# Kernel optimization log

Measured on AMD Instinct MI355X. Metric: run time of the kernel, lower is better.

The kernel has to match this reference:

```python
import math
import jax, jax.numpy as jnp
import numpy as np

S, B, H = 2048, 1, 4096
NH, HD = 32, 128          # heads, head dim
ROT = HD // 2             # rotary dim per 2D-RoPE half = 64


def rotate_half(x):
    x1, x2 = jnp.split(x, 2, axis=-1)
    return jnp.concatenate([-x2, x1], axis=-1)


def rope_tables(seq_len, dim, base=10000.0):
    inv_freq = 1.0 / (base ** (jnp.arange(0, dim, 2, dtype=jnp.float32) / dim))
    freqs = jnp.arange(seq_len, dtype=jnp.float32)[:, None] * inv_freq[None, :]
    emb = jnp.concatenate([freqs, freqs], axis=-1)  # [S, dim]
    return jnp.cos(emb), jnp.sin(emb)


def apply_rope(q, k, cos, sin, pos):
    # q,k: [S,B,NH,ROT]; pos: [S,B] -> gather cos/sin per token
    c = cos[pos][:, :, None, :]  # [S,B,1,ROT]
    s = sin[pos][:, :, None, :]
    return q * c + rotate_half(q) * s, k * c + rotate_half(k) * s


def setup_inputs() -> dict:
    key = jax.random.key(0)
    ks = jax.random.split(key, 5)
    hidden_states = jax.random.normal(ks[0], (S, B, H), dtype=jnp.float32)
    pos = jnp.arange(S, dtype=jnp.int64 if jax.config.jax_enable_x64 else jnp.int32)
    position_ids = jnp.stack([pos, pos])[None]  # [B=1, 2, S]
    attention_mask = jnp.triu(jnp.ones((S, S), dtype=bool), k=1)[None, None]  # True = masked
    scale = 0.02
    wqkv = jax.random.normal(ks[1], (3 * H, H), dtype=jnp.float32) * scale
    bqkv = jax.random.normal(ks[2], (3 * H,), dtype=jnp.float32) * scale
    wdense = jax.random.normal(ks[3], (H, H), dtype=jnp.float32) * scale
    bdense = jax.random.normal(ks[4], (H,), dtype=jnp.float32) * scale
    return {"hidden_states": hidden_states, "position_ids": position_ids,
            "attention_mask": attention_mask, "wqkv": wqkv, "bqkv": bqkv,
            "wdense": wdense, "bdense": bdense, "layer_id": 1}


def reference(hidden_states, position_ids, attention_mask, wqkv, bqkv, wdense, bdense, layer_id):
    s, b, h = hidden_states.shape
    # fused QKV projection: [S,B,NH,3*HD]
    mixed = (jnp.einsum('sbh,oh->sbo', hidden_states, wqkv) + bqkv).reshape(s, b, NH, 3 * HD)
    q, k, v = jnp.split(mixed, 3, axis=-1)  # each [S,B,NH,HD]

    # 2D RoPE: split head dim in half, rotate each half with its own position ids
    q1, q2 = jnp.split(q, 2, axis=-1)
    k1, k2 = jnp.split(k, 2, axis=-1)
    cos, sin = rope_tables(s, ROT)
    pos = position_ids[:, 0, :].T       # [S,B]
    block_pos = position_ids[:, 1, :].T  # [S,B]
    q1, k1 = apply_rope(q1, k1, cos, sin, pos)
    q2, k2 = apply_rope(q2, k2, cos, sin, block_pos)
    q = jnp.concatenate([q1, q2], axis=-1)
    k = jnp.concatenate([k1, k2], axis=-1)

    # layer-scaled attention (ChatGLM style)
    coeff = float(layer_id + 1)
    q = q / (math.sqrt(HD) * coeff)
    scores = jnp.einsum('sbhd,tbhd->bhst', q, k)  # [B,NH,S,S]
    scores = jnp.where(attention_mask, jnp.float32(-10000.0), scores)
    scores = scores.astype(jnp.float32) * coeff
    probs = jax.nn.softmax(scores, axis=-1).astype(q.dtype)
    context = jnp.einsum('bhst,tbhd->sbhd', probs, v).reshape(s, b, h)

    out = jnp.einsum('sbh,oh->sbo', context, wdense) + bdense
    return out
```

## Files before the change

### kernel.cpp

```cpp
#include <hip/hip_runtime.h>

typedef unsigned short u16;
typedef unsigned int u32;
typedef __attribute__((ext_vector_type(4))) float f32x4;
typedef __attribute__((ext_vector_type(8))) short bf16x8;
typedef __attribute__((ext_vector_type(2))) unsigned int u32x2;

#define S_LEN 2048
#define NHEAD 32
#define HDD 128
#define HID 4096
#define N_QKV 12288
#define KDIM 4096
#define RS 12288

__device__ __forceinline__ u16 f2bf(float f) {
  u32 u = __builtin_bit_cast(u32, f);
  u = (u + 0x7FFFu + ((u >> 16) & 1u)) >> 16;
  return (u16)u;
}
__device__ __forceinline__ float bf2f(u16 h) {
  u32 u = ((u32)h) << 16;
  return __builtin_bit_cast(float, u);
}

__device__ __forceinline__ void gl2lds16(const void* g, void* l) {
  __builtin_amdgcn_global_load_lds(
      (const __attribute__((address_space(1))) u32*)g,
      (__attribute__((address_space(3))) u32*)l, 16, 0, 0);
}

#define FULL_BAR()                          \
  {                                         \
    asm volatile("" ::: "memory");          \
    __builtin_amdgcn_s_barrier();           \
    asm volatile("" ::: "memory");          \
  }

__global__ __launch_bounds__(256) void cvt3_kernel(const float* __restrict__ s0, u16* __restrict__ d0, int n0,
                                                   const float* __restrict__ s1, u16* __restrict__ d1, int n1,
                                                   const float* __restrict__ s2, u16* __restrict__ d2, int n2,
                                                   float* __restrict__ cos_t, float* __restrict__ sin_t) {
  int i = blockIdx.x * blockDim.x + threadIdx.x;
  if (i < S_LEN * 32) {
    int s = i >> 5, ii = i & 31;
    float invf = expf(-0.28782313662425572f * (float)ii);
    float a = (float)s * invf;
    cos_t[i] = cosf(a);
    sin_t[i] = sinf(a);
  }
  int st = gridDim.x * blockDim.x;
  int ntot = n0 + n1 + n2;
  for (; i < ntot; i += st) {
    const float* s;
    u16* d;
    int j = i;
    if (j < n0) {
      s = s0; d = d0;
    } else if (j < n0 + n1) {
      j -= n0; s = s1; d = d1;
    } else {
      j -= n0 + n1; s = s2; d = d2;
    }
    float4 v = ((const float4*)s)[j];
    u32x2 o;
    o.x = (u32)f2bf(v.x) | ((u32)f2bf(v.y) << 16);
    o.y = (u32)f2bf(v.z) | ((u32)f2bf(v.w) << 16);
    ((u32x2*)d)[j] = o;
  }
}

__global__ __launch_bounds__(256) void rope_kernel(u16* __restrict__ mixed,
                                                   const int* __restrict__ pid,
                                                   const float* __restrict__ cos_t,
                                                   const float* __restrict__ sin_t) {
  int idx = blockIdx.x * blockDim.x + threadIdx.x;
  const int total = 2 * NHEAD * S_LEN * 2 * 8;
  if (idx >= total) return;
  int j = idx & 7;
  int half = (idx >> 3) & 1;
  int s = (idx >> 4) & (S_LEN - 1);
  int h = (idx >> 15) & (NHEAD - 1);
  int qk = idx >> 20;
  int i0 = j * 4;
  int p = pid[half * S_LEN + s];
  float4 c4 = *(const float4*)(cos_t + p * 32 + i0);
  float4 s4 = *(const float4*)(sin_t + p * 32 + i0);
  u16* base = mixed + (size_t)s * RS + h * 384 + qk * 128 + half * 64 + i0;
  ushort4 x1v = *(const ushort4*)(base);
  ushort4 x2v = *(const ushort4*)(base + 32);
  float sc = qk ? 1.0f : 0.08838834764831845f;
  ushort4 o1, o2;
  {
    float x1 = bf2f(x1v.x), x2 = bf2f(x2v.x);
    o1.x = f2bf((x1 * c4.x - x2 * s4.x) * sc);
    o2.x = f2bf((x2 * c4.x + x1 * s4.x) * sc);
  }
  {
    float x1 = bf2f(x1v.y), x2 = bf2f(x2v.y);
    o1.y = f2bf((x1 * c4.y - x2 * s4.y) * sc);
    o2.y = f2bf((x2 * c4.y + x1 * s4.y) * sc);
  }
  {
    float x1 = bf2f(x1v.z), x2 = bf2f(x2v.z);
    o1.z = f2bf((x1 * c4.z - x2 * s4.z) * sc);
    o2.z = f2bf((x2 * c4.z + x1 * s4.z) * sc);
  }
  {
    float x1 = bf2f(x1v.w), x2 = bf2f(x2v.w);
    o1.w = f2bf((x1 * c4.w - x2 * s4.w) * sc);
    o2.w = f2bf((x2 * c4.w + x1 * s4.w) * sc);
  }
  *(ushort4*)(base) = o1;
  *(ushort4*)(base + 32) = o2;
}

template <int NW, int EPI>
__global__ __launch_bounds__(512, 2) void gemmK(const u16* __restrict__ A,
                                                const u16* __restrict__ B,
                                                const float* __restrict__ bias, int N, int NTt,
                                                u16* __restrict__ outb, float* __restrict__ outf) {
  constexpr int BN = 32 * NW;
  constexpr int NLB = NW / 2;
  constexpr int BSUB = BN * 64;
  constexpr int BUFSZ = 32768 + 2 * BSUB;
  __shared__ __align__(16) char lds[2][BUFSZ];

  const int tid = threadIdx.x;
  const int lane = tid & 63, w = tid >> 6;
  const int l15 = lane & 15, g = lane >> 4;
  const int wm = w >> 1, wn = w & 1;

  int perx = gridDim.x >> 3;
  int npx = perx >> 3;
  int x = blockIdx.x & 7, loc = blockIdx.x >> 3;
  int mb = loc & 7, nb = x * npx + (loc >> 3);
  const int bm = mb * 256, bn = nb * BN;

  f32x4 acc[4][NW];
  f32x4 z4 = {0.f, 0.f, 0.f, 0.f};
#pragma unroll
  for (int mi = 0; mi < 4; ++mi)
#pragma unroll
    for (int ni = 0; ni < NW; ++ni) acc[mi][ni] = z4;

  const size_t K2 = (size_t)KDIM * 2;

  const char* gA[2];
#pragma unroll
  for (int j = 0; j < 2; ++j) {
    int slot = j * 512 + tid;
    int line = slot >> 3;
    int sl = (slot & 7) ^ (line & 7);
    int row = 2 * line + (sl >> 2);
    int colb = (sl & 3) * 16;
    gA[j] = (const char*)A + (size_t)(bm + row) * K2 + colb;
  }
  const char* gB[NLB];
#pragma unroll
  for (int j = 0; j < NLB; ++j) {
    int n_ = j * 512 + tid;
    int kkj = (n_ >= 128 * NW) ? 1 : 0;
    int m_ = n_ - kkj * 128 * NW;
    int line = m_ >> 3;
    int sl = (m_ & 7) ^ (line & 7);
    int row = 2 * line + (sl >> 2);
    int colb = (sl & 3) * 16;
    gB[j] = (const char*)B + (size_t)(bn + row) * K2 + kkj * 64 + colb;
  }
  const int ldst = w * 1024;

#define ISSUE_A(t, kk)                                                        \
  {                                                                           \
    char* Lb = lds[(t) & 1] + (kk) * 16384;                                   \
    gl2lds16(gA[0] + (size_t)(t) * 128 + (kk) * 64, Lb + ldst);               \
    gl2lds16(gA[1] + (size_t)(t) * 128 + (kk) * 64, Lb + 8192 + ldst);        \
  }
#define ISSUE_B(t)                                                            \
  {                                                                           \
    char* Lb = lds[(t) & 1] + 32768;                                          \
    _Pragma("unroll")                                                         \
    for (int j = 0; j < NLB; ++j)                                             \
      gl2lds16(gB[j] + (size_t)(t) * 128, Lb + j * 8192 + ldst);              \
  }

  int offA[4], offB[2][NW];
#pragma unroll
  for (int mi = 0; mi < 4; ++mi) {
    int r = wm * 64 + mi * 16 + l15;
    int line = r >> 1;
    int sl = (((r & 1) << 2) + g) ^ (line & 7);
    offA[mi] = line * 128 + sl * 16;
  }
#pragma unroll
  for (int kk = 0; kk < 2; ++kk)
#pragma unroll
    for (int ni = 0; ni < NW; ++ni) {
      int r = wn * (16 * NW) + ni * 16 + l15;
      int line = r >> 1;
      int sl = (((r & 1) << 2) + g) ^ (line & 7);
      offB[kk][ni] = 32768 + kk * BSUB + line * 128 + sl * 16;
    }

  ISSUE_A(0, 0);
  ISSUE_B(0);
  ISSUE_A(0, 1);
  asm volatile("s_waitcnt vmcnt(2)" ::: "memory");
  FULL_BAR();

  for (int kt = 0; kt < NTt; ++kt) {
    const char* buf = lds[kt & 1];
    const bool pf = (kt + 1) < NTt;
    bf16x8 a[4], b[NW];
#pragma unroll
    for (int mi = 0; mi < 4; ++mi) a[mi] = *(const bf16x8*)(buf + offA[mi]);
#pragma unroll
    for (int ni = 0; ni < NW; ++ni) b[ni] = *(const bf16x8*)(buf + offB[0][ni]);
    if (pf) {
      ISSUE_A(kt + 1, 0);
      ISSUE_B(kt + 1);
      asm volatile("s_waitcnt vmcnt(%0)" ::"i"(2 + NLB) : "memory");
    } else {
      asm volatile("s_waitcnt vmcnt(0)" ::: "memory");
    }
    FULL_BAR();
    __builtin_amdgcn_s_setprio(1);
#pragma unroll
    for (int mi = 0; mi < 4; ++mi)
#pragma unroll
      for (int ni = 0; ni < NW; ++ni)
        acc[mi][ni] = __builtin_amdgcn_mfma_f32_16x16x32_bf16(a[mi], b[ni], acc[mi][ni], 0, 0, 0);
    __builtin_amdgcn_s_setprio(0);
#pragma unroll
    for (int mi = 0; mi < 4; ++mi) a[mi] = *(const bf16x8*)(buf + 16384 + offA[mi]);
#pragma unroll
    for (int ni = 0; ni < NW; ++ni) b[ni] = *(const bf16x8*)(buf + offB[1][ni]);
    if (pf) {
      ISSUE_A(kt + 1, 1);
      asm volatile("s_waitcnt vmcnt(2)" ::: "memory");
    }
    FULL_BAR();
    __builtin_amdgcn_s_setprio(1);
#pragma unroll
    for (int mi = 0; mi < 4; ++mi)
#pragma unroll
      for (int ni = 0; ni < NW; ++ni)
        acc[mi][ni] = __builtin_amdgcn_mfma_f32_16x16x32_bf16(a[mi], b[ni], acc[mi][ni], 0, 0, 0);
    __builtin_amdgcn_s_setprio(0);
  }
#undef ISSUE_A
#undef ISSUE_B

#pragma unroll
  for (int ni = 0; ni < NW; ++ni) {
    int n = bn + wn * (16 * NW) + ni * 16 + l15;
    float bv = bias[n];
    if (EPI == 0) {
#pragma unroll
      for (int mi = 0; mi < 4; ++mi) {
        int m0 = bm + wm * 64 + mi * 16 + 4 * g;
#pragma unroll
        for (int rr = 0; rr < 4; ++rr)
          outb[(size_t)(m0 + rr) * N + n] = f2bf(acc[mi][ni][rr] + bv);
      }
    } else {
#pragma unroll
      for (int mi = 0; mi < 4; ++mi) {
        int m0 = bm + wm * 64 + mi * 16 + 4 * g;
#pragma unroll
        for (int rr = 0; rr < 4; ++rr) outf[(size_t)(m0 + rr) * N + n] = acc[mi][ni][rr] + bv;
      }
    }
  }
}

__global__ __launch_bounds__(256) void attn_kernel(const u16* __restrict__ mixed,
                                                   u16* __restrict__ ctx) {
  __shared__ __align__(16) u16 Ksh[32 * 136];
  __shared__ __align__(16) u16 Vsh[128 * 32];
  __shared__ __align__(16) u16 Pt[4][16 * 40];

  int tid = threadIdx.x;
  int lane = tid & 63, w = tid >> 6;
  int lane15 = lane & 15, g = lane >> 4;

  int bpair = blockIdx.x & 15;
  int h = blockIdx.x >> 4;

  const u16* qp = mixed + (size_t)h * 384;
  const u16* kp = mixed + (size_t)h * 384 + 128;
  const u16* vp = mixed + (size_t)h * 384 + 256;

  int krow = tid >> 3, kc = (tid & 7) * 16;
  int a_ = tid & 15, b_ = tid >> 4;
  f32x4 z4 = {0.f, 0.f, 0.f, 0.f};

  for (int pass = 0; pass < 2; ++pass) {
    int qi = pass ? (31 - bpair) : bpair;
    int qbase = qi * 64;
    int qrow = qbase + w * 16 + lane15;
    int ntiles = 2 * qi + 2;

    bf16x8 qf[4];
    const u16* qptr = qp + (size_t)qrow * RS + g * 8;
#pragma unroll
    for (int d0 = 0; d0 < 4; ++d0) qf[d0] = *(const bf16x8*)(qptr + d0 * 32);

    f32x4 pv[8];
#pragma unroll
    for (int db = 0; db < 8; ++db) pv[db] = z4;
    float m_run = -1e30f, l_run = 0.0f;

    for (int t = 0; t < ntiles; ++t) {
      int kb0 = t * 32;
      __syncthreads();
      {
        const bf16x8* src = (const bf16x8*)(kp + (size_t)(kb0 + krow) * RS + kc);
        bf16x8 x0 = src[0], x1 = src[1];
        *(bf16x8*)(Ksh + krow * 136 + kc) = x0;
        *(bf16x8*)(Ksh + krow * 136 + kc + 8) = x1;
        int k0 = 2 * a_, d0 = 8 * b_;
        bf16x8 r0 = *(const bf16x8*)(vp + (size_t)(kb0 + k0) * RS + d0);
        bf16x8 r1 = *(const bf16x8*)(vp + (size_t)(kb0 + k0 + 1) * RS + d0);
#pragma unroll
        for (int jj = 0; jj < 8; ++jj) {
          int d = d0 + jj;
          u32 val = (u32)(u16)r0[jj] | ((u32)(u16)r1[jj] << 16);
          *(u32*)(Vsh + d * 32 + (((k0 >> 3) ^ (d & 3)) << 3) + (k0 & 7)) = val;
        }
      }
      __syncthreads();

      f32x4 sa0 = z4, sa1 = z4;
#pragma unroll
      for (int d0 = 0; d0 < 4; ++d0) {
        bf16x8 k0f = *(const bf16x8*)(Ksh + lane15 * 136 + d0 * 32 + g * 8);
        bf16x8 k1f = *(const bf16x8*)(Ksh + (16 + lane15) * 136 + d0 * 32 + g * 8);
        sa0 = __builtin_amdgcn_mfma_f32_16x16x32_bf16(k0f, qf[d0], sa0, 0, 0, 0);
        sa1 = __builtin_amdgcn_mfma_f32_16x16x32_bf16(k1f, qf[d0], sa1, 0, 0, 0);
      }
      float s[8];
#pragma unroll
      for (int rr = 0; rr < 4; ++rr) {
        int kg0 = kb0 + 4 * g + rr;
        int kg1 = kb0 + 16 + 4 * g + rr;
        s[rr] = (kg0 > qrow) ? -1e30f : sa0[rr];
        s[4 + rr] = (kg1 > qrow) ? -1e30f : sa1[rr];
      }
      float mx = s[0];
#pragma unroll
      for (int i2 = 1; i2 < 8; ++i2) mx = fmaxf(mx, s[i2]);
      mx = fmaxf(mx, __shfl_xor(mx, 16));
      mx = fmaxf(mx, __shfl_xor(mx, 32));
      float mnew = fmaxf(m_run, mx);
      float fac = exp2f((m_run - mnew) * 1.4426950408889634f);
      float p[8], psum = 0.f;
#pragma unroll
      for (int i2 = 0; i2 < 8; ++i2) {
        p[i2] = exp2f((s[i2] - mnew) * 1.4426950408889634f);
        psum += p[i2];
      }
      psum += __shfl_xor(psum, 16);
      psum += __shfl_xor(psum, 32);
      l_run = l_run * fac + psum;
      m_run = mnew;
#pragma unroll
      for (int db = 0; db < 8; ++db) pv[db] *= fac;

      u32 w0 = (u32)f2bf(p[0]) | ((u32)f2bf(p[1]) << 16);
      u32 w1 = (u32)f2bf(p[2]) | ((u32)f2bf(p[3]) << 16);
      u32 w2 = (u32)f2bf(p[4]) | ((u32)f2bf(p[5]) << 16);
      u32 w3 = (u32)f2bf(p[6]) | ((u32)f2bf(p[7]) << 16);
      u32x2 pa, pb;
      pa.x = w0; pa.y = w1; pb.x = w2; pb.y = w3;
      *(u32x2*)(&Pt[w][lane15 * 40 + 4 * g]) = pa;
      *(u32x2*)(&Pt[w][lane15 * 40 + 16 + 4 * g]) = pb;
      asm volatile("s_waitcnt lgkmcnt(0)" ::: "memory");
      bf16x8 pfrag = *(const bf16x8*)(&Pt[w][lane15 * 40 + 8 * g]);

#pragma unroll
      for (int db = 0; db < 8; ++db) {
        int d = db * 16 + lane15;
        bf16x8 vf = *(const bf16x8*)(Vsh + d * 32 + ((g ^ (d & 3)) << 3));
        pv[db] = __builtin_amdgcn_mfma_f32_16x16x32_bf16(vf, pfrag, pv[db], 0, 0, 0);
      }
    }

    float inv = 1.0f / l_run;
#pragma unroll
    for (int db = 0; db < 8; ++db) {
      ushort4 o;
      o.x = f2bf(pv[db][0] * inv);
      o.y = f2bf(pv[db][1] * inv);
      o.z = f2bf(pv[db][2] * inv);
      o.w = f2bf(pv[db][3] * inv);
      *(ushort4*)(ctx + (size_t)qrow * HID + h * HDD + db * 16 + 4 * g) = o;
    }
    __syncthreads();
  }
}

extern "C" void kernel_launch(void* const* d_in, const int* in_sizes, int n_in,
                              void* d_out, int out_size, void* d_ws, size_t ws_size,
                              hipStream_t stream) {
  const float* hidden = (const float*)d_in[0];
  const int* pid = (const int*)d_in[1];
  const float* wqkv = (const float*)d_in[3];
  const float* bqkv = (const float*)d_in[4];
  const float* wdense = (const float*)d_in[5];
  const float* bdense = (const float*)d_in[6];
  float* out = (float*)d_out;

  char* ws = (char*)d_ws;
  u16* W1 = (u16*)ws;
  u16* W2 = (u16*)(ws + 100663296);
  u16* X = (u16*)(ws + 134217728);
  u16* mixed = (u16*)(ws + 150994944);
  u16* ctx = (u16*)(ws + 201326592);
  float* cos_t = (float*)(ws + 218103808);
  float* sin_t = (float*)(ws + 218365952);

  cvt3_kernel<<<dim3(2048), dim3(256), 0, stream>>>(
      wqkv, W1, N_QKV * KDIM / 4, wdense, W2, HID * KDIM / 4, hidden, X, S_LEN * HID / 4,
      cos_t, sin_t);

  gemmK<6, 0><<<dim3(512), dim3(512), 0, stream>>>(
      X, W1, bqkv, N_QKV, 64, mixed, nullptr);

  rope_kernel<<<dim3(8192), dim3(256), 0, stream>>>(mixed, pid, cos_t, sin_t);

  attn_kernel<<<dim3(512), dim3(256), 0, stream>>>(mixed, ctx);

  gemmK<4, 1><<<dim3(256), dim3(512), 0, stream>>>(
      ctx, W2, bdense, HID, 64, nullptr, out);
}
```

Before: 500.5 us.

## Fuse RoPE into attention loads and add dedicated larger-tile QKV GEMM

Removes the standalone RoPE kernel and applies the rotary embedding (and query scaling) inside the attention kernel: queries are rotated in registers after loading, and keys are rotated while staging each tile into shared memory. The QKV projection switches to a new GEMM with 256x384 tiles, 8 waves, triple-buffered LDS and grouped block ordering, replacing the generic gemmK instance. This removes one read-modify-write pass over Q and K and one launch, and aims for more reuse per tile in the largest GEMM. In exchange, K is rotated again by every query block that reads it, and the larger tile raises register pressure and leaves fewer blocks for the grid.

```diff
diff --git a/kernel.cpp b/kernel.cpp
--- a/kernel.cpp
+++ b/kernel.cpp
@@ -70,49 +70,139 @@
   }
 }
 
-__global__ __launch_bounds__(256) void rope_kernel(u16* __restrict__ mixed,
-                                                   const int* __restrict__ pid,
-                                                   const float* __restrict__ cos_t,
-                                                   const float* __restrict__ sin_t) {
-  int idx = blockIdx.x * blockDim.x + threadIdx.x;
-  const int total = 2 * NHEAD * S_LEN * 2 * 8;
-  if (idx >= total) return;
-  int j = idx & 7;
-  int half = (idx >> 3) & 1;
-  int s = (idx >> 4) & (S_LEN - 1);
-  int h = (idx >> 15) & (NHEAD - 1);
-  int qk = idx >> 20;
-  int i0 = j * 4;
-  int p = pid[half * S_LEN + s];
-  float4 c4 = *(const float4*)(cos_t + p * 32 + i0);
-  float4 s4 = *(const float4*)(sin_t + p * 32 + i0);
-  u16* base = mixed + (size_t)s * RS + h * 384 + qk * 128 + half * 64 + i0;
-  ushort4 x1v = *(const ushort4*)(base);
-  ushort4 x2v = *(const ushort4*)(base + 32);
-  float sc = qk ? 1.0f : 0.08838834764831845f;
-  ushort4 o1, o2;
-  {
-    float x1 = bf2f(x1v.x), x2 = bf2f(x2v.x);
-    o1.x = f2bf((x1 * c4.x - x2 * s4.x) * sc);
-    o2.x = f2bf((x2 * c4.x + x1 * s4.x) * sc);
-  }
-  {
-    float x1 = bf2f(x1v.y), x2 = bf2f(x2v.y);
-    o1.y = f2bf((x1 * c4.y - x2 * s4.y) * sc);
-    o2.y = f2bf((x2 * c4.y + x1 * s4.y) * sc);
-  }
-  {
-    float x1 = bf2f(x1v.z), x2 = bf2f(x2v.z);
-    o1.z = f2bf((x1 * c4.z - x2 * s4.z) * sc);
-    o2.z = f2bf((x2 * c4.z + x1 * s4.z) * sc);
-  }
-  {
-    float x1 = bf2f(x1v.w), x2 = bf2f(x2v.w);
-    o1.w = f2bf((x1 * c4.w - x2 * s4.w) * sc);
-    o2.w = f2bf((x2 * c4.w + x1 * s4.w) * sc);
-  }
-  *(ushort4*)(base) = o1;
-  *(ushort4*)(base + 32) = o2;
+__global__ __launch_bounds__(512, 2) void gemmQ(const u16* __restrict__ A,
+                                                const u16* __restrict__ B,
+                                                const float* __restrict__ bias,
+                                                u16* __restrict__ outb) {
+  __shared__ __align__(16) char lds[3][40960];
+
+  const int tid = threadIdx.x;
+  const int lane = tid & 63, w = tid >> 6;
+  const int l15 = lane & 15, g = lane >> 4;
+  const int wm = w >> 2, wn = w & 3;
+
+  int x = blockIdx.x & 7, loc = blockIdx.x >> 3;
+  int mb = loc & 7, nb = x * 4 + (loc >> 3);
+  const int bm = mb * 256, bn = nb * 384;
+
+  f32x4 acc[8][6];
+  f32x4 z4 = {0.f, 0.f, 0.f, 0.f};
+#pragma unroll
+  for (int mi = 0; mi < 8; ++mi)
+#pragma unroll
+    for (int ni = 0; ni < 6; ++ni) acc[mi][ni] = z4;
+
+  const size_t K2 = (size_t)KDIM * 2;
+
+  const char* gA[2];
+#pragma unroll
+  for (int j = 0; j < 2; ++j) {
+    int slot = j * 512 + tid;
+    int line = slot >> 3;
+    int sl = (slot & 7) ^ (line & 7);
+    int row = 2 * line + (sl >> 2);
+    int colb = (sl & 3) * 16;
+    gA[j] = (const char*)A + (size_t)(bm + row) * K2 + colb;
+  }
+  const char* gB[3];
+#pragma unroll
+  for (int j = 0; j < 3; ++j) {
+    int slot = j * 512 + tid;
+    int line = slot >> 3;
+    int sl = (slot & 7) ^ (line & 7);
+    int row = 2 * line + (sl >> 2);
+    int colb = (sl & 3) * 16;
+    gB[j] = (const char*)B + (size_t)(bn + row) * K2 + colb;
+  }
+  const int ldst = w * 1024;
+
+#define QIA(t, bi)                                                  \
+  {                                                                 \
+    char* Lb = lds[bi];                                             \
+    gl2lds16(gA[0] + (size_t)(t) * 64, Lb + ldst);                  \
+    gl2lds16(gA[1] + (size_t)(t) * 64, Lb + 8192 + ldst);           \
+  }
+#define QIB(t, bi)                                                  \
+  {                                                                 \
+    char* Lb = lds[bi] + 16384;                                     \
+    _Pragma("unroll")                                               \
+    for (int j = 0; j < 3; ++j)                                     \
+      gl2lds16(gB[j] + (size_t)(t) * 64, Lb + j * 8192 + ldst);     \
+  }
+
+  int offA[8], offB[6];
+#pragma unroll
+  for (int mi = 0; mi < 8; ++mi) {
+    int r = wm * 128 + mi * 16 + l15;
+    int line = r >> 1;
+    int sl = (((r & 1) << 2) + g) ^ (line & 7);
+    offA[mi] = line * 128 + sl * 16;
+  }
+#pragma unroll
+  for (int ni = 0; ni < 6; ++ni) {
+    int r = wn * 96 + ni * 16 + l15;
+    int line = r >> 1;
+    int sl = (((r & 1) << 2) + g) ^ (line & 7);
+    offB[ni] = 16384 + line * 128 + sl * 16;
+  }
+
+  QIA(0, 0); QIB(0, 0);
+  QIA(1, 1); QIB(1, 1);
+  asm volatile("s_waitcnt vmcnt(5)" ::: "memory");
+  FULL_BAR();
+
+  int cur = 0, nx2 = 2;
+  for (int kt = 0; kt < 128; ++kt) {
+    const char* buf = lds[cur];
+    const bool pf = (kt + 2) < 128;
+    bf16x8 a[4], b[6];
+#pragma unroll
+    for (int mi = 0; mi < 4; ++mi) a[mi] = *(const bf16x8*)(buf + offA[mi]);
+#pragma unroll
+    for (int ni = 0; ni < 6; ++ni) b[ni] = *(const bf16x8*)(buf + offB[ni]);
+    if (pf) QIA(kt + 2, nx2);
+    FULL_BAR();
+    __builtin_amdgcn_s_setprio(1);
+#pragma unroll
+    for (int mi = 0; mi < 4; ++mi)
+#pragma unroll
+      for (int ni = 0; ni < 6; ++ni)
+        acc[mi][ni] = __builtin_amdgcn_mfma_f32_16x16x32_bf16(a[mi], b[ni], acc[mi][ni], 0, 0, 0);
+    __builtin_amdgcn_s_setprio(0);
+#pragma unroll
+    for (int mi = 0; mi < 4; ++mi) a[mi] = *(const bf16x8*)(buf + offA[4 + mi]);
+    if (pf) {
+      QIB(kt + 2, nx2);
+      asm volatile("s_waitcnt vmcnt(5)" ::: "memory");
+    } else if (kt == 126) {
+      asm volatile("s_waitcnt vmcnt(0)" ::: "memory");
+    }
+    FULL_BAR();
+    __builtin_amdgcn_s_setprio(1);
+#pragma unroll
+    for (int mi = 0; mi < 4; ++mi)
+#pragma unroll
+      for (int ni = 0; ni < 6; ++ni)
+        acc[4 + mi][ni] = __builtin_amdgcn_mfma_f32_16x16x32_bf16(a[mi], b[ni], acc[4 + mi][ni], 0, 0, 0);
+    __builtin_amdgcn_s_setprio(0);
+    cur = (cur + 1 == 3) ? 0 : cur + 1;
+    nx2 = (nx2 + 1 == 3) ? 0 : nx2 + 1;
+  }
+#undef QIA
+#undef QIB
+
+#pragma unroll
+  for (int ni = 0; ni < 6; ++ni) {
+    int n = bn + wn * 96 + ni * 16 + l15;
+    float bv = bias[n];
+#pragma unroll
+    for (int mi = 0; mi < 8; ++mi) {
+      int m0 = bm + wm * 128 + mi * 16 + 4 * g;
+#pragma unroll
+      for (int rr = 0; rr < 4; ++rr)
+        outb[(size_t)(m0 + rr) * N_QKV + n] = f2bf(acc[mi][ni][rr] + bv);
+    }
+  }
 }
 
 template <int NW, int EPI>
@@ -275,6 +365,9 @@
 }
 
 __global__ __launch_bounds__(256) void attn_kernel(const u16* __restrict__ mixed,
+                                                   const int* __restrict__ pid,
+                                                   const float* __restrict__ cos_t,
+                                                   const float* __restrict__ sin_t,
                                                    u16* __restrict__ ctx) {
   __shared__ __align__(16) u16 Ksh[32 * 136];
   __shared__ __align__(16) u16 Vsh[128 * 32];
@@ -291,9 +384,14 @@
   const u16* kp = mixed + (size_t)h * 384 + 128;
   const u16* vp = mixed + (size_t)h * 384 + 256;
 
-  int krow = tid >> 3, kc = (tid & 7) * 16;
+  int krow = tid >> 3;
+  int kc8 = tid & 7;
+  int ke0 = (kc8 & 3) * 8 + (kc8 >> 2) * 64;
+  int khalf = (kc8 >> 2);
+  int ki0 = ke0 & 31;
   int a_ = tid & 15, b_ = tid >> 4;
   f32x4 z4 = {0.f, 0.f, 0.f, 0.f};
+  const float QSC = 0.08838834764831845f;
 
   for (int pass = 0; pass < 2; ++pass) {
     int qi = pass ? (31 - bpair) : bpair;
@@ -305,6 +403,34 @@
     const u16* qptr = qp + (size_t)qrow * RS + g * 8;
 #pragma unroll
     for (int d0 = 0; d0 < 4; ++d0) qf[d0] = *(const bf16x8*)(qptr + d0 * 32);
+    {
+      int p1 = pid[qrow], p2 = pid[S_LEN + qrow];
+      float4 c1a = *(const float4*)(cos_t + p1 * 32 + g * 8);
+      float4 c1b = *(const float4*)(cos_t + p1 * 32 + g * 8 + 4);
+      float4 s1a = *(const float4*)(sin_t + p1 * 32 + g * 8);
+      float4 s1b = *(const float4*)(sin_t + p1 * 32 + g * 8 + 4);
+      float4 c2a = *(const float4*)(cos_t + p2 * 32 + g * 8);
+      float4 c2b = *(const float4*)(cos_t + p2 * 32 + g * 8 + 4);
+      float4 s2a = *(const float4*)(sin_t + p2 * 32 + g * 8);
+      float4 s2b = *(const float4*)(sin_t + p2 * 32 + g * 8 + 4);
+      float cc[8], ss[8], dd[8], tt[8];
+#pragma unroll
+      for (int j = 0; j < 4; ++j) {
+        cc[j] = ((const float*)&c1a)[j]; cc[4 + j] = ((const float*)&c1b)[j];
+        ss[j] = ((const float*)&s1a)[j]; ss[4 + j] = ((const float*)&s1b)[j];
+        dd[j] = ((const float*)&c2a)[j]; dd[4 + j] = ((const float*)&c2b)[j];
+        tt[j] = ((const float*)&s2a)[j]; tt[4 + j] = ((const float*)&s2b)[j];
+      }
+#pragma unroll
+      for (int j = 0; j < 8; ++j) {
+        float x1 = bf2f((u16)qf[0][j]), x2 = bf2f((u16)qf[1][j]);
+        qf[0][j] = (short)f2bf((x1 * cc[j] - x2 * ss[j]) * QSC);
+        qf[1][j] = (short)f2bf((x2 * cc[j] + x1 * ss[j]) * QSC);
+        float y1 = bf2f((u16)qf[2][j]), y2 = bf2f((u16)qf[3][j]);
+        qf[2][j] = (short)f2bf((y1 * dd[j] - y2 * tt[j]) * QSC);
+        qf[3][j] = (short)f2bf((y2 * dd[j] + y1 * tt[j]) * QSC);
+      }
+    }
 
     f32x4 pv[8];
 #pragma unroll
@@ -315,10 +441,25 @@
       int kb0 = t * 32;
       __syncthreads();
       {
-        const bf16x8* src = (const bf16x8*)(kp + (size_t)(kb0 + krow) * RS + kc);
-        bf16x8 x0 = src[0], x1 = src[1];
-        *(bf16x8*)(Ksh + krow * 136 + kc) = x0;
-        *(bf16x8*)(Ksh + krow * 136 + kc + 8) = x1;
+        int p = pid[khalf * S_LEN + kb0 + krow];
+        const u16* rowp = kp + (size_t)(kb0 + krow) * RS;
+        bf16x8 x1 = *(const bf16x8*)(rowp + ke0);
+        bf16x8 x2 = *(const bf16x8*)(rowp + ke0 + 32);
+        float4 ca = *(const float4*)(cos_t + p * 32 + ki0);
+        float4 cb = *(const float4*)(cos_t + p * 32 + ki0 + 4);
+        float4 sa = *(const float4*)(sin_t + p * 32 + ki0);
+        float4 sb = *(const float4*)(sin_t + p * 32 + ki0 + 4);
+        bf16x8 o1, o2;
+#pragma unroll
+        for (int j = 0; j < 8; ++j) {
+          float c = (j < 4) ? ((const float*)&ca)[j] : ((const float*)&cb)[j - 4];
+          float s = (j < 4) ? ((const float*)&sa)[j] : ((const float*)&sb)[j - 4];
+          float v1 = bf2f((u16)x1[j]), v2 = bf2f((u16)x2[j]);
+          o1[j] = (short)f2bf(v1 * c - v2 * s);
+          o2[j] = (short)f2bf(v2 * c + v1 * s);
+        }
+        *(bf16x8*)(Ksh + krow * 136 + ke0) = o1;
+        *(bf16x8*)(Ksh + krow * 136 + ke0 + 32) = o2;
         int k0 = 2 * a_, d0 = 8 * b_;
         bf16x8 r0 = *(const bf16x8*)(vp + (size_t)(kb0 + k0) * RS + d0);
         bf16x8 r1 = *(const bf16x8*)(vp + (size_t)(kb0 + k0 + 1) * RS + d0);
@@ -424,12 +565,9 @@
       wqkv, W1, N_QKV * KDIM / 4, wdense, W2, HID * KDIM / 4, hidden, X, S_LEN * HID / 4,
       cos_t, sin_t);
 
-  gemmK<6, 0><<<dim3(512), dim3(512), 0, stream>>>(
-      X, W1, bqkv, N_QKV, 64, mixed, nullptr);
-
-  rope_kernel<<<dim3(8192), dim3(256), 0, stream>>>(mixed, pid, cos_t, sin_t);
-
-  attn_kernel<<<dim3(512), dim3(256), 0, stream>>>(mixed, ctx);
+  gemmQ<<<dim3(256), dim3(512), 0, stream>>>(X, W1, bqkv, mixed);
+
+  attn_kernel<<<dim3(512), dim3(256), 0, stream>>>(mixed, pid, cos_t, sin_t, ctx);
 
   gemmK<4, 1><<<dim3(256), dim3(512), 0, stream>>>(
       ctx, W2, bdense, HID, 64, nullptr, out);
```

Result: no change. 497.3 us (-0.6%).
